# Performance work log

Measured on AMD Instinct MI355X. Metric: run time of the kernel, lower is better.

The kernel has to match this reference:

```python
import jax, jax.numpy as jnp
import numpy as np

NUM_CODES = 1024
CODE_DIM = 64
EMA_DECAY = 0.99
COMMIT_W = 0.25
EPS = 1e-5
B = 262144


def setup_inputs() -> dict:
    key = jax.random.key(0)
    k1, k2, k3, k4 = jax.random.split(key, 4)
    z = jax.random.normal(k1, (B, CODE_DIM), dtype=jnp.float32)
    weight = jax.random.normal(k2, (NUM_CODES, CODE_DIM), dtype=jnp.float32)
    ema_cluster_size = jax.random.uniform(k3, (NUM_CODES,), dtype=jnp.float32)
    ema_embed_sum = jax.random.normal(k4, (NUM_CODES, CODE_DIM), dtype=jnp.float32)
    return {"z": z, "weight": weight, "ema_cluster_size": ema_cluster_size,
            "ema_embed_sum": ema_embed_sum}


def reference(z, weight, ema_cluster_size, ema_embed_sum):
    # Squared Euclidean distances (argmin equivalent to cdist argmin)
    # d2[b,k] = ||z_b||^2 - 2 z_b . w_k + ||w_k||^2
    z2 = jnp.sum(z * z, axis=-1, keepdims=True)          # (B, 1)
    w2 = jnp.sum(weight * weight, axis=-1)               # (K,)
    d2 = z2 - 2.0 * (z @ weight.T) + w2[None, :]         # (B, K)
    indices = jnp.argmin(d2, axis=-1)                    # (B,)
    z_q = weight[indices]                                # gather with OLD weights

    # EMA codebook update (training, ema_update=True)
    ones = jnp.ones((z.shape[0],), dtype=z.dtype)
    cluster_size = jax.ops.segment_sum(ones, indices, num_segments=NUM_CODES)
    embed_sum = jax.ops.segment_sum(z, indices, num_segments=NUM_CODES)
    new_cs = EMA_DECAY * ema_cluster_size + (1.0 - EMA_DECAY) * cluster_size
    new_es = EMA_DECAY * ema_embed_sum + (1.0 - EMA_DECAY) * embed_sum
    n = jnp.sum(new_cs)
    smoothed = (new_cs + EPS) / (n + NUM_CODES * EPS) * n
    new_weight = new_es / smoothed[:, None]

    # commitment loss (z detached in torch; pure value here)
    vq_loss = COMMIT_W * jnp.mean((z - z_q) ** 2)

    # straight-through estimator
    z_q_st = z + jax.lax.stop_gradient(z_q - z)
    return z_q_st, indices, vq_loss, new_cs, new_es, new_weight
```

## Files before the change

### kernel.cpp

```cpp
#include <hip/hip_runtime.h>

typedef __attribute__((ext_vector_type(8))) short bf16x8;
typedef __attribute__((ext_vector_type(4))) float f32x4;

#define B_ROWS 262144
#define K_CODES 1024
#define DIM 64
#define DELTA 0.015f

#define OUT_ZQ 0
#define OUT_IDX 16777216
#define OUT_LOSS 17039360
#define OUT_NEWCS 17039361
#define OUT_NEWES 17040385
#define OUT_NEWW 17105921

#define WS_LOSS   0
#define WS_QCOUNT 1
#define WS_W2     16
#define WS_SMOOTH 1040
#define WS_WHIP   2064
#define WS_WLOP   34832
#define WS_CPART  67600
#define WS_EPART  100368
#define WS_MINI   2197520
#define WS_QUEUE  2459664

static __device__ __forceinline__ unsigned short f2bf(float x) {
    unsigned u = __float_as_uint(x);
    return (unsigned short)((u + 0x7fffu + ((u >> 16) & 1u)) >> 16);
}
static __device__ __forceinline__ float bf2f(unsigned short u) {
    return __uint_as_float(((unsigned)u) << 16);
}

static __device__ __forceinline__ void cvt_frag(const float* zrow, bf16x8& hi, bf16x8& lo) {
    float4 f0 = *(const float4*)zrow;
    float4 f1 = *(const float4*)(zrow + 4);
    float tf[8] = {f0.x, f0.y, f0.z, f0.w, f1.x, f1.y, f1.z, f1.w};
#pragma unroll
    for (int j = 0; j < 8; ++j) {
        unsigned short h = f2bf(tf[j]);
        hi[j] = (short)h;
        lo[j] = (short)f2bf(tf[j] - bf2f(h));
    }
}

__global__ __launch_bounds__(256) void vq_prep(const float* __restrict__ w,
                                               float* __restrict__ ws) {
    int b = blockIdx.x, tid = threadIdx.x;
    if (b < 4) {
        int k = b * 256 + tid;
        const float4* w4 = (const float4*)(w + (size_t)k * DIM);
        float s = 0.f;
#pragma unroll
        for (int j = 0; j < 16; ++j) {
            float4 v = w4[j];
            s += v.x * v.x + v.y * v.y + v.z * v.z + v.w * v.w;
        }
        ws[WS_W2 + k] = s;
    } else {
        int i = (b - 4) * 256 + tid;
        int p = i & 1023, c = i >> 10;
        int code = c * 128 + ((p >> 7) << 4) + (p & 15);
        int octet = ((p >> 6) & 1) * 4 + ((p >> 4) & 3);
        const float* src = w + (size_t)code * DIM + octet * 8;
        float4 f0 = *(const float4*)src;
        float4 f1 = *(const float4*)(src + 4);
        float tf[8] = {f0.x, f0.y, f0.z, f0.w, f1.x, f1.y, f1.z, f1.w};
        bf16x8 hv, lv;
#pragma unroll
        for (int j = 0; j < 8; ++j) {
            unsigned short hb = f2bf(tf[j]);
            hv[j] = (short)hb;
            lv[j] = (short)f2bf(tf[j] - bf2f(hb));
        }
        ((bf16x8*)(ws + WS_WHIP))[i] = hv;
        ((bf16x8*)(ws + WS_WLOP))[i] = lv;
    }
}

__global__ __launch_bounds__(256)
__attribute__((amdgpu_waves_per_eu(3, 4))) void vq_screen_kernel(
    const float* __restrict__ z, float* __restrict__ ws) {
    __shared__ float lds_w2[K_CODES];

    int tid = threadIdx.x;
    int l = tid & 63, wave = tid >> 6;
    int m = l & 15, q = l >> 4;

    *(float4*)&lds_w2[tid * 4] = ((const float4*)(ws + WS_W2))[tid];

    int rowbase = blockIdx.x * 128 + wave * 32;
    bf16x8 ahi[2][2], alo[2][2];
#pragma unroll
    for (int g = 0; g < 2; ++g) {
        const float* zr = z + (size_t)(rowbase + g * 16 + m) * DIM + q * 8;
        cvt_frag(zr, ahi[g][0], alo[g][0]);
        cvt_frag(zr + 32, ahi[g][1], alo[g][1]);
    }

    float mv[8], m2[8];
    int mi[8];
#pragma unroll
    for (int v = 0; v < 8; ++v) { mv[v] = 3.4e38f; m2[v] = 3.4e38f; mi[v] = 0; }

    const bf16x8* __restrict__ gh = (const bf16x8*)(ws + WS_WHIP);
    const bf16x8* __restrict__ gl = (const bf16x8*)(ws + WS_WLOP);

    __syncthreads();

    for (int cch = 0; cch < 8; ++cch) {
#pragma unroll 2
        for (int tg = 0; tg < 8; ++tg) {
            int gi = cch * 1024 + tg * 128 + l;
            bf16x8 bh0 = gh[gi];
            bf16x8 bh1 = gh[gi + 64];
            bf16x8 bl0 = gl[gi];
            bf16x8 bl1 = gl[gi + 64];
            int cg = cch * 128 + tg * 16 + m;
            float w2v = lds_w2[cg];
#pragma unroll
            for (int g = 0; g < 2; ++g) {
                f32x4 acc = {0.f, 0.f, 0.f, 0.f};
                acc = __builtin_amdgcn_mfma_f32_16x16x32_bf16(alo[g][0], bh0, acc, 0, 0, 0);
                acc = __builtin_amdgcn_mfma_f32_16x16x32_bf16(ahi[g][0], bl0, acc, 0, 0, 0);
                acc = __builtin_amdgcn_mfma_f32_16x16x32_bf16(alo[g][1], bh1, acc, 0, 0, 0);
                acc = __builtin_amdgcn_mfma_f32_16x16x32_bf16(ahi[g][1], bl1, acc, 0, 0, 0);
                acc = __builtin_amdgcn_mfma_f32_16x16x32_bf16(ahi[g][0], bh0, acc, 0, 0, 0);
                acc = __builtin_amdgcn_mfma_f32_16x16x32_bf16(ahi[g][1], bh1, acc, 0, 0, 0);
#pragma unroll
                for (int r = 0; r < 4; ++r) {
                    int v = g * 4 + r;
                    float d = fmaf(acc[r], -2.0f, w2v);
                    m2[v] = fminf(m2[v], fmaxf(mv[v], d));
                    bool lt = d < mv[v];
                    mv[v] = fminf(mv[v], d);
                    mi[v] = lt ? cg : mi[v];
                }
            }
        }
    }

#pragma unroll
    for (int o = 1; o < 16; o <<= 1) {
#pragma unroll
        for (int v = 0; v < 8; ++v) {
            float ov = __shfl_xor(mv[v], o, 64);
            float ov2 = __shfl_xor(m2[v], o, 64);
            int oi = __shfl_xor(mi[v], o, 64);
            float nm2 = fminf(fminf(m2[v], ov2), fmaxf(mv[v], ov));
            bool take = (ov < mv[v]) || (ov == mv[v] && oi < mi[v]);
            mv[v] = take ? ov : mv[v];
            mi[v] = take ? oi : mi[v];
            m2[v] = nm2;
        }
    }
    if (m == 0) {
#pragma unroll
        for (int v = 0; v < 8; ++v) {
            int g = v >> 2, r = v & 3;
            int row = rowbase + g * 16 + q * 4 + r;
            bool amb = (m2[v] - mv[v] <= DELTA);
            ((int*)ws)[WS_MINI + row] = mi[v] | (amb ? 0x80000000 : 0);
        }
    }
}

__global__ __launch_bounds__(256) void vq_gather_kernel(
    const float* __restrict__ z, const float* __restrict__ w,
    float* __restrict__ ws, float* __restrict__ out) {
    __shared__ float lred[4];
    int tid = threadIdx.x;
    int lane = tid & 63, wave = tid >> 6;
    int rsub = lane >> 4;
    int d4 = lane & 15;
    int wavebase = blockIdx.x * 256 + wave * 64;

    int encv[16];
#pragma unroll
    for (int s = 0; s < 16; ++s)
        encv[s] = ((const int*)ws)[WS_MINI + wavebase + s * 4 + rsub];

    float lsum = 0.f;
#pragma unroll
    for (int s = 0; s < 16; ++s) {
        int row = wavebase + s * 4 + rsub;
        int enc = encv[s];
        if (enc >= 0) {
            float4 x = ((const float4*)(z + (size_t)row * DIM))[d4];
            float4 qv = ((const float4*)(w + (size_t)enc * DIM))[d4];
            float4 st;
            st.x = x.x + (qv.x - x.x);
            st.y = x.y + (qv.y - x.y);
            st.z = x.z + (qv.z - x.z);
            st.w = x.w + (qv.w - x.w);
            ((float4*)(out + OUT_ZQ + (size_t)row * DIM))[d4] = st;
            float e0 = x.x - qv.x, e1 = x.y - qv.y, e2 = x.z - qv.z, e3 = x.w - qv.w;
            lsum += e0 * e0;
            lsum += e1 * e1;
            lsum += e2 * e2;
            lsum += e3 * e3;
            if (d4 == 0) out[OUT_IDX + row] = (float)enc;
        } else if (d4 == 0) {
            int pos = atomicAdd((int*)ws + WS_QCOUNT, 1);
            ((int*)ws)[WS_QUEUE + pos] = row;
        }
    }
#pragma unroll
    for (int o = 32; o; o >>= 1) lsum += __shfl_down(lsum, o, 64);
    if (lane == 0) lred[wave] = lsum;
    __syncthreads();
    if (tid == 0) atomicAdd(ws + WS_LOSS, lred[0] + lred[1] + lred[2] + lred[3]);
}

__global__ __launch_bounds__(256) void vq_fixup_kernel(
    const float* __restrict__ z, const float* __restrict__ w,
    float* __restrict__ ws, float* __restrict__ out) {
    const float* __restrict__ w2 = ws + WS_W2;
    int count = ((const int*)ws)[WS_QCOUNT];
    int lane = threadIdx.x & 63;
    int wv = (blockIdx.x * 256 + threadIdx.x) >> 6;
    int nw = (gridDim.x * 256) >> 6;
    for (int qi = wv; qi < count; qi += nw) {
        int row = ((const int*)ws)[WS_QUEUE + qi];
        const float* zr = z + (size_t)row * DIM;
        float zloc[DIM];
#pragma unroll
        for (int d = 0; d < DIM; ++d) zloc[d] = zr[d];
        float z2 = 0.f;
#pragma unroll
        for (int d = 0; d < DIM; ++d) z2 = fmaf(zloc[d], zloc[d], z2);
        float best = 3.4e38f;
        int bi = 0;
        for (int i = 0; i < 16; ++i) {
            int c = i * 64 + lane;
            const float* wr = w + (size_t)c * DIM;
            float a = 0.f;
#pragma unroll
            for (int d = 0; d < DIM; ++d) a = fmaf(zloc[d], wr[d], a);
            float dd = (z2 - 2.f * a) + w2[c];
            if (dd < best) { best = dd; bi = c; }
        }
#pragma unroll
        for (int o = 1; o < 64; o <<= 1) {
            float ov = __shfl_xor(best, o, 64);
            int oi = __shfl_xor(bi, o, 64);
            if (ov < best || (ov == best && oi < bi)) { best = ov; bi = oi; }
        }
        float x = zr[lane];
        float qv = w[(size_t)bi * DIM + lane];
        out[OUT_ZQ + (size_t)row * DIM + lane] = x + (qv - x);
        float e = x - qv;
        float s = e * e;
#pragma unroll
        for (int o = 32; o; o >>= 1) s += __shfl_down(s, o, 64);
        if (lane == 0) {
            out[OUT_IDX + row] = (float)bi;
            atomicAdd(ws + WS_LOSS, s);
        }
    }
}

__global__ __launch_bounds__(1024) void vq_embed_kernel(
    const float* __restrict__ z, const float* __restrict__ idx_f,
    float* __restrict__ ws) {
    __shared__ float eacc[128 * DIM];
    __shared__ float ecnt[128];
    __shared__ int lists[16][256];
    int b = blockIdx.x;
    int cs = b & 7, rs = b >> 3;
    float lo = (float)(cs * 128), hi = lo + 128.f;
    int tid = threadIdx.x;
    int wave = tid >> 6, lane = tid & 63;

#pragma unroll
    for (int j = 0; j < 8; ++j) eacc[j * 1024 + tid] = 0.f;
    if (tid < 128) ecnt[tid] = 0.f;
    __syncthreads();

    const float4* idx4 = (const float4*)idx_f;
    unsigned long long lanebits = (1ull << lane) - 1ull;
    for (int it = 0; it < 2; ++it) {
        int base = rs * 8192 + wave * 512 + it * 256;
        float4 f = idx4[(base >> 2) + lane];
        int cnt = 0;
#pragma unroll
        for (int c = 0; c < 4; ++c) {
            float fv = (c == 0) ? f.x : (c == 1) ? f.y : (c == 2) ? f.z : f.w;
            bool match = (fv >= lo && fv < hi);
            unsigned long long mmask = __ballot(match);
            if (match) {
                int pos = cnt + __popcll(mmask & lanebits);
                int row = base + 4 * lane + c;
                int local = (int)fv - cs * 128;
                lists[wave][pos] = (row << 7) | local;
                atomicAdd(&ecnt[local], 1.f);
            }
            cnt += __popcll(mmask);
        }
        int j = 0;
        for (; j + 4 <= cnt; j += 4) {
            int e0 = lists[wave][j], e1 = lists[wave][j + 1];
            int e2 = lists[wave][j + 2], e3 = lists[wave][j + 3];
            float v0 = z[(size_t)(e0 >> 7) * DIM + lane];
            float v1 = z[(size_t)(e1 >> 7) * DIM + lane];
            float v2 = z[(size_t)(e2 >> 7) * DIM + lane];
            float v3 = z[(size_t)(e3 >> 7) * DIM + lane];
            atomicAdd(&eacc[(e0 & 127) * DIM + lane], v0);
            atomicAdd(&eacc[(e1 & 127) * DIM + lane], v1);
            atomicAdd(&eacc[(e2 & 127) * DIM + lane], v2);
            atomicAdd(&eacc[(e3 & 127) * DIM + lane], v3);
        }
        for (; j < cnt; ++j) {
            int e = lists[wave][j];
            float v = z[(size_t)(e >> 7) * DIM + lane];
            atomicAdd(&eacc[(e & 127) * DIM + lane], v);
        }
    }
    __syncthreads();
#pragma unroll
    for (int j = 0; j < 8; ++j)
        ws[WS_EPART + (size_t)b * 8192 + j * 1024 + tid] = eacc[j * 1024 + tid];
    if (tid < 128) ws[WS_CPART + b * 128 + tid] = ecnt[tid];
}

__global__ __launch_bounds__(1024) void vq_finalize1_kernel(
    const float* __restrict__ ema_cs, float* __restrict__ ws,
    float* __restrict__ out) {
    int k = threadIdx.x;
    int cs = k >> 7, local = k & 127;
    float c = 0.f;
#pragma unroll
    for (int rs = 0; rs < 32; ++rs) c += ws[WS_CPART + (rs * 8 + cs) * 128 + local];
    float nc = 0.99f * ema_cs[k] + 0.01f * c;
    out[OUT_NEWCS + k] = nc;

    float s = nc;
#pragma unroll
    for (int o = 32; o; o >>= 1) s += __shfl_down(s, o, 64);
    __shared__ float red[16];
    __shared__ float n_sh;
    if ((k & 63) == 0) red[k >> 6] = s;
    __syncthreads();
    if (k == 0) {
        float n = 0.f;
#pragma unroll
        for (int i = 0; i < 16; ++i) n += red[i];
        n_sh = n;
        out[OUT_LOSS] = 0.25f * (ws[WS_LOSS] / 16777216.0f);
    }
    __syncthreads();
    float n = n_sh;
    ws[WS_SMOOTH + k] = (nc + 1e-5f) / (n + 0.01024f) * n;
}

__global__ __launch_bounds__(256) void vq_finalize2_kernel(
    const float* __restrict__ ema_es, const float* __restrict__ ws,
    float* __restrict__ out) {
    int i = blockIdx.x * 256 + threadIdx.x;
    int code = i >> 6, dim = i & 63;
    int cs = code >> 7, local = code & 127;
    float e = 0.f;
#pragma unroll
    for (int rs = 0; rs < 32; ++rs)
        e += ws[WS_EPART + (size_t)(rs * 8 + cs) * 8192 + local * DIM + dim];
    float es = 0.99f * ema_es[i] + 0.01f * e;
    out[OUT_NEWES + i] = es;
    out[OUT_NEWW + i] = es / ws[WS_SMOOTH + code];
}

extern "C" void kernel_launch(void* const* d_in, const int* in_sizes, int n_in,
                              void* d_out, int out_size, void* d_ws, size_t ws_size,
                              hipStream_t stream) {
    const float* z = (const float*)d_in[0];
    const float* weight = (const float*)d_in[1];
    const float* ema_cs = (const float*)d_in[2];
    const float* ema_es = (const float*)d_in[3];
    float* out = (float*)d_out;
    float* ws = (float*)d_ws;

    hipMemsetAsync(ws, 0, 64, stream);
    vq_prep<<<36, 256, 0, stream>>>(weight, ws);
    vq_screen_kernel<<<B_ROWS / 128, 256, 0, stream>>>(z, ws);
    vq_gather_kernel<<<B_ROWS / 256, 256, 0, stream>>>(z, weight, ws, out);
    vq_fixup_kernel<<<256, 256, 0, stream>>>(z, weight, ws, out);
    vq_embed_kernel<<<256, 1024, 0, stream>>>(z, out + OUT_IDX, ws);
    vq_finalize1_kernel<<<1, 1024, 0, stream>>>(ema_cs, ws, out);
    vq_finalize2_kernel<<<256, 256, 0, stream>>>(ema_es, ws, out);
}
```

Before: 419.9 us.

## Pack code index into score mantissa and transpose MFMA to cut argmin overhead

The screening kernel now computes a max-score form (z·w − ½‖w‖²) with the ‖w‖² term preloaded as the MFMA accumulator init, and swaps operand order so each lane holds four codes for one row. The code index is packed into the low 10 mantissa bits of each score, so a plain fmax tracks the best code and a top-2 tracker needs no separate index compare or select. This removes the per-element fma, compare and select work and shrinks the cross-lane reduction from four shuffle stages over eight values to two stages over two values. In exchange the scores lose precision to the packed bits, and the ambiguity threshold is widened so rows near a tie are still sent to the exact recheck path.

```diff
diff --git a/kernel.cpp b/kernel.cpp
--- a/kernel.cpp
+++ b/kernel.cpp
@@ -6,7 +6,7 @@
 #define B_ROWS 262144
 #define K_CODES 1024
 #define DIM 64
-#define DELTA 0.015f
+#define SDELTA 0.03f
 
 #define OUT_ZQ 0
 #define OUT_IDX 16777216
@@ -83,27 +83,34 @@
 __global__ __launch_bounds__(256)
 __attribute__((amdgpu_waves_per_eu(3, 4))) void vq_screen_kernel(
     const float* __restrict__ z, float* __restrict__ ws) {
-    __shared__ float lds_w2[K_CODES];
+    __shared__ float lds_w2h[K_CODES];
 
     int tid = threadIdx.x;
     int l = tid & 63, wave = tid >> 6;
     int m = l & 15, q = l >> 4;
 
-    *(float4*)&lds_w2[tid * 4] = ((const float4*)(ws + WS_W2))[tid];
+    {
+        float4 wv = ((const float4*)(ws + WS_W2))[tid];
+        float4 hv;
+        hv.x = -0.5f * wv.x;
+        hv.y = -0.5f * wv.y;
+        hv.z = -0.5f * wv.z;
+        hv.w = -0.5f * wv.w;
+        *(float4*)&lds_w2h[tid * 4] = hv;
+    }
 
     int rowbase = blockIdx.x * 128 + wave * 32;
-    bf16x8 ahi[2][2], alo[2][2];
+    bf16x8 zhi[2][2], zlo[2][2];
 #pragma unroll
     for (int g = 0; g < 2; ++g) {
         const float* zr = z + (size_t)(rowbase + g * 16 + m) * DIM + q * 8;
-        cvt_frag(zr, ahi[g][0], alo[g][0]);
-        cvt_frag(zr + 32, ahi[g][1], alo[g][1]);
-    }
-
-    float mv[8], m2[8];
-    int mi[8];
-#pragma unroll
-    for (int v = 0; v < 8; ++v) { mv[v] = 3.4e38f; m2[v] = 3.4e38f; mi[v] = 0; }
+        cvt_frag(zr, zhi[g][0], zlo[g][0]);
+        cvt_frag(zr + 32, zhi[g][1], zlo[g][1]);
+    }
+
+    float kv[2], k2[2];
+    kv[0] = kv[1] = -3.4e38f;
+    k2[0] = k2[1] = -3.4e38f;
 
     const bf16x8* __restrict__ gh = (const bf16x8*)(ws + WS_WHIP);
     const bf16x8* __restrict__ gl = (const bf16x8*)(ws + WS_WLOP);
@@ -118,51 +125,47 @@
             bf16x8 bh1 = gh[gi + 64];
             bf16x8 bl0 = gl[gi];
             bf16x8 bl1 = gl[gi + 64];
-            int cg = cch * 128 + tg * 16 + m;
-            float w2v = lds_w2[cg];
+            unsigned cbase = (unsigned)(cch * 128 + tg * 16 + q * 4);
+            f32x4 cinit = *(const f32x4*)&lds_w2h[cbase];
 #pragma unroll
             for (int g = 0; g < 2; ++g) {
-                f32x4 acc = {0.f, 0.f, 0.f, 0.f};
-                acc = __builtin_amdgcn_mfma_f32_16x16x32_bf16(alo[g][0], bh0, acc, 0, 0, 0);
-                acc = __builtin_amdgcn_mfma_f32_16x16x32_bf16(ahi[g][0], bl0, acc, 0, 0, 0);
-                acc = __builtin_amdgcn_mfma_f32_16x16x32_bf16(alo[g][1], bh1, acc, 0, 0, 0);
-                acc = __builtin_amdgcn_mfma_f32_16x16x32_bf16(ahi[g][1], bl1, acc, 0, 0, 0);
-                acc = __builtin_amdgcn_mfma_f32_16x16x32_bf16(ahi[g][0], bh0, acc, 0, 0, 0);
-                acc = __builtin_amdgcn_mfma_f32_16x16x32_bf16(ahi[g][1], bh1, acc, 0, 0, 0);
-#pragma unroll
-                for (int r = 0; r < 4; ++r) {
-                    int v = g * 4 + r;
-                    float d = fmaf(acc[r], -2.0f, w2v);
-                    m2[v] = fminf(m2[v], fmaxf(mv[v], d));
-                    bool lt = d < mv[v];
-                    mv[v] = fminf(mv[v], d);
-                    mi[v] = lt ? cg : mi[v];
-                }
+                f32x4 acc = cinit;
+                acc = __builtin_amdgcn_mfma_f32_16x16x32_bf16(bh0, zlo[g][0], acc, 0, 0, 0);
+                acc = __builtin_amdgcn_mfma_f32_16x16x32_bf16(bl0, zhi[g][0], acc, 0, 0, 0);
+                acc = __builtin_amdgcn_mfma_f32_16x16x32_bf16(bh1, zlo[g][1], acc, 0, 0, 0);
+                acc = __builtin_amdgcn_mfma_f32_16x16x32_bf16(bl1, zhi[g][1], acc, 0, 0, 0);
+                acc = __builtin_amdgcn_mfma_f32_16x16x32_bf16(bh0, zhi[g][0], acc, 0, 0, 0);
+                acc = __builtin_amdgcn_mfma_f32_16x16x32_bf16(bh1, zhi[g][1], acc, 0, 0, 0);
+                float a0 = __uint_as_float((__float_as_uint(acc[0]) & 0xFFFFFC00u) | cbase);
+                float a1 = __uint_as_float((__float_as_uint(acc[1]) & 0xFFFFFC00u) | (cbase + 1u));
+                float a2 = __uint_as_float((__float_as_uint(acc[2]) & 0xFFFFFC00u) | (cbase + 2u));
+                float a3 = __uint_as_float((__float_as_uint(acc[3]) & 0xFFFFFC00u) | (cbase + 3u));
+                float m01 = fmaxf(a0, a1), n01 = fminf(a0, a1);
+                float m23 = fmaxf(a2, a3), n23 = fminf(a2, a3);
+                float top = fmaxf(m01, m23);
+                float sec = fmaxf(fmaxf(fminf(m01, m23), n01), n23);
+                k2[g] = fmaxf(fmaxf(k2[g], sec), fminf(kv[g], top));
+                kv[g] = fmaxf(kv[g], top);
             }
         }
     }
 
 #pragma unroll
-    for (int o = 1; o < 16; o <<= 1) {
-#pragma unroll
-        for (int v = 0; v < 8; ++v) {
-            float ov = __shfl_xor(mv[v], o, 64);
-            float ov2 = __shfl_xor(m2[v], o, 64);
-            int oi = __shfl_xor(mi[v], o, 64);
-            float nm2 = fminf(fminf(m2[v], ov2), fmaxf(mv[v], ov));
-            bool take = (ov < mv[v]) || (ov == mv[v] && oi < mi[v]);
-            mv[v] = take ? ov : mv[v];
-            mi[v] = take ? oi : mi[v];
-            m2[v] = nm2;
-        }
-    }
-    if (m == 0) {
-#pragma unroll
-        for (int v = 0; v < 8; ++v) {
-            int g = v >> 2, r = v & 3;
-            int row = rowbase + g * 16 + q * 4 + r;
-            bool amb = (m2[v] - mv[v] <= DELTA);
-            ((int*)ws)[WS_MINI + row] = mi[v] | (amb ? 0x80000000 : 0);
+    for (int o = 16; o < 64; o <<= 1) {
+#pragma unroll
+        for (int g = 0; g < 2; ++g) {
+            float ov = __shfl_xor(kv[g], o, 64);
+            float ov2 = __shfl_xor(k2[g], o, 64);
+            k2[g] = fmaxf(fmaxf(k2[g], ov2), fminf(kv[g], ov));
+            kv[g] = fmaxf(kv[g], ov);
+        }
+    }
+    if (q == 0) {
+#pragma unroll
+        for (int g = 0; g < 2; ++g) {
+            int code = (int)(__float_as_uint(kv[g]) & 1023u);
+            bool amb = (kv[g] - k2[g]) <= SDELTA;
+            ((int*)ws)[WS_MINI + rowbase + g * 16 + m] = code | (amb ? 0x80000000 : 0);
         }
     }
 }
```

Result: slower. 538.7 us (+28.3%).
